# Kernel optimization log

Measured on AMD Instinct MI355X. Metric: run time of the kernel, lower is better.

The kernel has to match this reference:

```python
import jax, jax.numpy as jnp
import numpy as np

F_IN, F_H, N_A, N_B = 256, 512, 40, 4
N_GRAPHS, NODES_PER_GRAPH = 4096, 32
N_NODES = N_GRAPHS * NODES_PER_GRAPH
D_OUT = N_B + N_B * N_A  # 164
BN_EPS = 1e-5


def setup_inputs() -> dict:
    key = jax.random.key(0)
    ks = jax.random.split(key, 8)
    X = jax.random.normal(ks[0], (N_NODES, F_IN), dtype=jnp.float32)
    # fixed-size graphs: consistent NX / NX_rep pair
    NX = jnp.full((N_GRAPHS,), NODES_PER_GRAPH, dtype=jnp.int64)
    NX_rep = jnp.repeat(jnp.arange(N_GRAPHS, dtype=jnp.int64), NODES_PER_GRAPH)
    def kaiming(k, fo, fi):
        return jax.random.normal(k, (fo, fi), dtype=jnp.float32) * np.float32(1.0 / np.sqrt(fi))
    return {
        "X": X, "NX": NX, "NX_rep": NX_rep,
        "W_h": kaiming(ks[1], F_H, 2 * F_IN),          # linear_h (no bias)
        "g_h": jnp.ones((F_H,), jnp.float32), "b_h": jnp.zeros((F_H,), jnp.float32),
        "W_ht": kaiming(ks[2], F_H, F_IN),              # linear_h_t (no bias)
        "g_ht": jnp.ones((F_H,), jnp.float32), "b_ht": jnp.zeros((F_H,), jnp.float32),
        "W_x": kaiming(ks[3], D_OUT, F_H) * 0.1,        # linear_x
        "b_x": jnp.zeros((D_OUT,), jnp.float32),
        "W_xt": kaiming(ks[4], 1, F_H) * 0.1,           # linear_x_t
        "b_xt": jnp.zeros((1,), jnp.float32),
    }


def _batchnorm(x, gamma, beta):
    # BatchNorm1d in training mode: batch statistics, biased variance
    mean = jnp.mean(x, axis=0)
    var = jnp.var(x, axis=0)
    return (x - mean) * jax.lax.rsqrt(var + BN_EPS) * gamma + beta


def reference(X, NX, NX_rep, W_h, g_h, b_h, W_ht, g_ht, b_ht, W_x, b_x, W_xt, b_xt):
    n_graphs = NX.shape[0]
    # graph-level mean pooling via segment sum  -> [G, F_in]
    X_end = jax.ops.segment_sum(X, NX_rep, num_segments=n_graphs) / NX[:, None].astype(X.dtype)
    # concat node features with gathered graph context -> [N, 2*F_in]
    Xc = jnp.concatenate([X, X_end[NX_rep]], axis=1)
    X_h = jax.nn.relu(_batchnorm(Xc @ W_h.T, g_h, b_h))          # [N, F_h]
    X_h_end = jax.nn.relu(_batchnorm(X_end @ W_ht.T, g_ht, b_ht))  # [G, F_h]
    X_x = jnp.exp(X_h @ W_x.T + b_x)                              # [N, D_OUT]
    X_x_end = jnp.exp(X_h_end @ W_xt.T + b_xt)                    # [G, 1]
    # segmented softmax denominator (per graph, over all nodes x D_OUT + end logit)
    X_sum = jnp.sum(jax.ops.segment_sum(X_x, NX_rep, num_segments=n_graphs),
                    axis=-1, keepdims=True) + X_x_end             # [G, 1]
    X_softmax = X_x / X_sum[NX_rep]                               # [N, D_OUT]
    X_softmax_end = X_x_end / X_sum                               # [G, 1]
    connect = X_softmax[:, :N_B]                                  # [N, N_B]
    append = X_softmax[:, N_B:].reshape(-1, N_A, N_B)             # [N, N_A, N_B]
    end = X_softmax_end.squeeze(-1)                               # [G]
    return (append, connect, end)
```

## Files before the change

kernel.cpp:

```cpp
#include <hip/hip_runtime.h>
#include <hip/hip_bf16.h>

typedef __hip_bfloat16 bf16;
typedef __attribute__((ext_vector_type(8))) short bf16x8;
typedef __attribute__((ext_vector_type(4))) float f32x4;

#define N_NODES   131072
#define N_GRAPHS  4096
#define FIN       256
#define FH        512
#define NPAD      176
#define NREAL     164

#define OFF_XB     0UL
#define OFF_XEND   67108864UL
#define OFF_XENDB  71303168UL
#define OFF_W1A    73400320UL
#define OFF_BCAT   73662464UL
#define OFF_WXB    74186752UL
#define OFF_CCAT   74366976UL
#define OFF_H      91144192UL
#define OFF_STATS  225361920UL
#define OFF_COEF   225370112UL
#define OFF_XXE    225378304UL

__device__ __forceinline__ void gld_lds16(const void* g, void* l) {
  __builtin_amdgcn_global_load_lds(
      (const __attribute__((address_space(1))) void*)g,
      (__attribute__((address_space(3))) void*)l, 16, 0, 0);
}

__device__ __forceinline__ float bf2f(unsigned short u) {
  unsigned int x = ((unsigned int)u) << 16; float f;
  __builtin_memcpy(&f, &x, 4); return f;
}
__device__ __forceinline__ unsigned short f2bf(float f) {
  bf16 h = __float2bfloat16(f); unsigned short u;
  __builtin_memcpy(&u, &h, 2); return u;
}

__global__ __launch_bounds__(256) void k_wcast(
    const float* __restrict__ W_h, const float* __restrict__ W_ht,
    const float* __restrict__ W_x,
    bf16* __restrict__ W1a, bf16* __restrict__ Bcat, bf16* __restrict__ Wxb)
{
  int i = blockIdx.x * 256 + threadIdx.x;
  if (i < 512 * 512) {
    int of = i >> 9, ic = i & 511;
    float v = W_h[i];
    if (ic < 256) W1a[of * 256 + ic] = __float2bfloat16(v);
    else          Bcat[of * 256 + (ic - 256)] = __float2bfloat16(v);
  }
  if (i < 512 * 256) Bcat[512 * 256 + i] = __float2bfloat16(W_ht[i]);
  if (i < NPAD * 512) {
    int n = i >> 9;
    Wxb[i] = (n < NREAL) ? __float2bfloat16(W_x[i]) : __float2bfloat16(0.f);
  }
}

__global__ __launch_bounds__(256) void k_xend(
    const float* __restrict__ X, const int* __restrict__ NX,
    bf16* __restrict__ Xb, float* __restrict__ X_end, bf16* __restrict__ X_endb)
{
  int g = blockIdx.x;
  int f = threadIdx.x;
  float s = 0.f;
  long base = (long)g * 32 * FIN + f;
  #pragma unroll 4
  for (int n = 0; n < 32; ++n) {
    float v = X[base + (long)n * FIN];
    s += v;
    Xb[base + (long)n * FIN] = __float2bfloat16(v);
  }
  float m = s / (float)NX[g];
  X_end[g * FIN + f] = m;
  X_endb[g * FIN + f] = __float2bfloat16(m);
}

template <int MODE>
__global__ __launch_bounds__(256, 2) void gemm_tn(
    const bf16* __restrict__ A, int lda,
    const bf16* __restrict__ B, int ldb, int K,
    const float* __restrict__ Cterm, int ldct,
    float* __restrict__ Cout, int ldc,
    bf16* __restrict__ Hout, int nblk)
{
  const int bid = blockIdx.x;
  const int blkM = bid / nblk, blkN = bid % nblk;
  const int tid = threadIdx.x;
  const int w = tid >> 6, lane = tid & 63;
  const int wm = w >> 1, wn = w & 1;

  __shared__ __align__(16) bf16 lA[128 * 32];
  __shared__ __align__(16) bf16 lB[128 * 32];

  f32x4 acc[4][4] = {};

  const int rS = lane >> 2;
  const int cS = (lane & 3) * 8;
  const long baseA = (long)blkM * 128;
  const long baseB = (long)blkN * 128;

  for (int kk = 0; kk < K; kk += 32) {
    #pragma unroll
    for (int c = 0; c < 2; ++c) {
      int chunk = 2 * w + c;
      gld_lds16(A + (baseA + chunk * 16 + rS) * lda + kk + cS, &lA[chunk * 16 * 32]);
      gld_lds16(B + (baseB + chunk * 16 + rS) * ldb + kk + cS, &lB[chunk * 16 * 32]);
    }
    __syncthreads();
    bf16x8 a8[4], b8[4];
    #pragma unroll
    for (int t = 0; t < 4; ++t) {
      a8[t] = *(const bf16x8*)&lA[(wm * 64 + t * 16 + (lane & 15)) * 32 + (lane >> 4) * 8];
      b8[t] = *(const bf16x8*)&lB[(wn * 64 + t * 16 + (lane & 15)) * 32 + (lane >> 4) * 8];
    }
    #pragma unroll
    for (int tm = 0; tm < 4; ++tm)
      #pragma unroll
      for (int tn = 0; tn < 4; ++tn)
        acc[tm][tn] = __builtin_amdgcn_mfma_f32_16x16x32_bf16(a8[tm], b8[tn], acc[tm][tn], 0, 0, 0);
    __syncthreads();
  }

  const int rowq = (lane >> 4) * 4;
  const int coll = lane & 15;
  #pragma unroll
  for (int tm = 0; tm < 4; ++tm)
    #pragma unroll
    for (int tn = 0; tn < 4; ++tn)
      #pragma unroll
      for (int r = 0; r < 4; ++r) {
        long row = baseA + wm * 64 + tm * 16 + rowq + r;
        int col = (int)baseB + wn * 64 + tn * 16 + coll;
        if (MODE == 0) {
          Cout[row * ldc + col] = acc[tm][tn][r];
        } else {
          int g = (int)(row >> 5);
          float h = acc[tm][tn][r] + Cterm[(long)g * ldct + col];
          Hout[row * FH + col] = __float2bfloat16(h);
        }
      }
}

__global__ __launch_bounds__(256) void k_stats_main(
    const bf16* __restrict__ H, float* __restrict__ s1, float* __restrict__ s2)
{
  long r0 = (long)blockIdx.x * 128;
  int tid = threadIdx.x;
  #pragma unroll
  for (int cc = 0; cc < 2; ++cc) {
    int c = tid + cc * 256;
    float a = 0.f, b = 0.f;
    for (int r = 0; r < 128; ++r) {
      float v = bf2f(*(const unsigned short*)&H[(r0 + r) * FH + c]);
      a += v; b += v * v;
    }
    atomicAdd(&s1[c], a); atomicAdd(&s2[c], b);
  }
}

__global__ __launch_bounds__(256) void k_stats_end(
    const float* __restrict__ Ccat, float* __restrict__ s1, float* __restrict__ s2)
{
  long r0 = (long)blockIdx.x * 64;
  int tid = threadIdx.x;
  #pragma unroll
  for (int cc = 0; cc < 2; ++cc) {
    int c = tid + cc * 256;
    float a = 0.f, b = 0.f;
    for (int r = 0; r < 64; ++r) {
      float v = Ccat[(r0 + r) * 1024 + 512 + c];
      a += v; b += v * v;
    }
    atomicAdd(&s1[c], a); atomicAdd(&s2[c], b);
  }
}

__global__ __launch_bounds__(256) void k_finalize(
    const float* __restrict__ s1, const float* __restrict__ s2,
    const float* __restrict__ gam, const float* __restrict__ bet,
    float invN, float* __restrict__ a_s, float* __restrict__ c_s)
{
  int c = blockIdx.x * 256 + threadIdx.x;
  if (c < FH) {
    float mean = s1[c] * invN;
    float var = s2[c] * invN - mean * mean;
    float a = gam[c] / sqrtf(var + 1e-5f);
    a_s[c] = a;
    c_s[c] = bet[c] - mean * a;
  }
}

__global__ __launch_bounds__(256) void k_xxend(
    const float* __restrict__ Ccat, const float* __restrict__ at,
    const float* __restrict__ ct, const float* __restrict__ Wxt,
    const float* __restrict__ bxt, float* __restrict__ Xxe)
{
  int w = threadIdx.x >> 6, lane = threadIdx.x & 63;
  int g = blockIdx.x * 4 + w;
  const float* h = Ccat + (long)g * 1024 + 512;
  float acc = 0.f;
  #pragma unroll
  for (int i = 0; i < 8; ++i) {
    int j = lane + i * 64;
    float x = fmaxf(at[j] * h[j] + ct[j], 0.f);
    acc += x * Wxt[j];
  }
  #pragma unroll
  for (int off = 32; off; off >>= 1) acc += __shfl_xor(acc, off);
  if (lane == 0) Xxe[g] = expf(acc + bxt[0]);
}

__global__ __launch_bounds__(256) void k_transform(
    bf16* __restrict__ H, const float* __restrict__ a_s, const float* __restrict__ c_s)
{
  long i = ((long)blockIdx.x * 256 + threadIdx.x) * 8;
  int c0 = (int)(i & 511);
  uint4 d = *(const uint4*)((const char*)H + i * 2);
  unsigned short* u = (unsigned short*)&d;
  #pragma unroll
  for (int t = 0; t < 8; ++t) {
    float v = bf2f(u[t]);
    v = fmaxf(a_s[c0 + t] * v + c_s[c0 + t], 0.f);
    u[t] = f2bf(v);
  }
  *(uint4*)((char*)H + i * 2) = d;
}

__global__ __launch_bounds__(256, 2) void gemm2_softmax(
    const bf16* __restrict__ A2, const bf16* __restrict__ Wxb,
    const float* __restrict__ b_x, const float* __restrict__ Xxe,
    float* __restrict__ outA, float* __restrict__ outC, float* __restrict__ outE)
{
  const int blk = blockIdx.x;
  const int tid = threadIdx.x;
  const int w = tid >> 6, lane = tid & 63;

  __shared__ __align__(16) bf16 lA[128 * 32];
  __shared__ __align__(16) bf16 lB[NPAD * 32];

  f32x4 acc[2][11] = {};
  const int rS = lane >> 2;
  const int cS = (lane & 3) * 8;
  const long baseRow = (long)blk * 128;

  for (int kk = 0; kk < FH; kk += 32) {
    #pragma unroll
    for (int c = 0; c < 2; ++c) {
      int chunk = 2 * w + c;
      gld_lds16(A2 + (baseRow + chunk * 16 + rS) * FH + kk + cS, &lA[chunk * 16 * 32]);
    }
    for (int o = w; o < 11; o += 4)
      gld_lds16(Wxb + (o * 16 + rS) * FH + kk + cS, &lB[o * 16 * 32]);
    __syncthreads();

    bf16x8 a8[2], b8[11];
    #pragma unroll
    for (int t = 0; t < 2; ++t)
      a8[t] = *(const bf16x8*)&lA[(w * 32 + t * 16 + (lane & 15)) * 32 + (lane >> 4) * 8];
    #pragma unroll
    for (int t = 0; t < 11; ++t)
      b8[t] = *(const bf16x8*)&lB[(t * 16 + (lane & 15)) * 32 + (lane >> 4) * 8];
    #pragma unroll
    for (int tm = 0; tm < 2; ++tm)
      #pragma unroll
      for (int tn = 0; tn < 11; ++tn)
        acc[tm][tn] = __builtin_amdgcn_mfma_f32_16x16x32_bf16(a8[tm], b8[tn], acc[tm][tn], 0, 0, 0);
    __syncthreads();
  }

  const int rowq = (lane >> 4) * 4;
  const int coll = lane & 15;
  const int g = blk * 4 + w;
  float psum = 0.f;
  #pragma unroll
  for (int tn = 0; tn < 11; ++tn) {
    int col = tn * 16 + coll;
    bool valid = col < NREAL;
    float bx = valid ? b_x[col] : 0.f;
    #pragma unroll
    for (int tm = 0; tm < 2; ++tm)
      #pragma unroll
      for (int r = 0; r < 4; ++r) {
        float p = valid ? expf(acc[tm][tn][r] + bx) : 0.f;
        acc[tm][tn][r] = p;
        psum += p;
      }
  }
  #pragma unroll
  for (int off = 32; off; off >>= 1) psum += __shfl_xor(psum, off);
  float Xe = Xxe[g];
  float inv = 1.0f / (psum + Xe);
  if (lane == 0) outE[g] = Xe * inv;

  #pragma unroll
  for (int tn = 0; tn < 11; ++tn) {
    int col = tn * 16 + coll;
    if (col >= NREAL) continue;
    #pragma unroll
    for (int tm = 0; tm < 2; ++tm)
      #pragma unroll
      for (int r = 0; r < 4; ++r) {
        long row = baseRow + w * 32 + tm * 16 + rowq + r;
        float v = acc[tm][tn][r] * inv;
        if (col >= 4) outA[row * 160 + (col - 4)] = v;
        else          outC[row * 4 + col] = v;
      }
  }
}

extern "C" void kernel_launch(void* const* d_in, const int* in_sizes, int n_in,
                              void* d_out, int out_size, void* d_ws, size_t ws_size,
                              hipStream_t stream)
{
  const float* X    = (const float*)d_in[0];
  const int*   NX   = (const int*)d_in[1];
  const float* W_h  = (const float*)d_in[3];
  const float* g_h  = (const float*)d_in[4];
  const float* b_h  = (const float*)d_in[5];
  const float* W_ht = (const float*)d_in[6];
  const float* g_ht = (const float*)d_in[7];
  const float* b_ht = (const float*)d_in[8];
  const float* W_x  = (const float*)d_in[9];
  const float* b_x  = (const float*)d_in[10];
  const float* W_xt = (const float*)d_in[11];
  const float* b_xt = (const float*)d_in[12];

  char* ws = (char*)d_ws;
  bf16*  Xb    = (bf16*)(ws + OFF_XB);
  float* X_end = (float*)(ws + OFF_XEND);
  bf16*  X_endb= (bf16*)(ws + OFF_XENDB);
  bf16*  W1a   = (bf16*)(ws + OFF_W1A);
  bf16*  Bcat  = (bf16*)(ws + OFF_BCAT);
  bf16*  Wxb   = (bf16*)(ws + OFF_WXB);
  float* Ccat  = (float*)(ws + OFF_CCAT);
  bf16*  H     = (bf16*)(ws + OFF_H);
  float* stats = (float*)(ws + OFF_STATS);
  float* s1m = stats, *s2m = stats + 512, *s1e = stats + 1024, *s2e = stats + 1536;
  float* coef  = (float*)(ws + OFF_COEF);
  float* a_s = coef, *c_s = coef + 512, *at_s = coef + 1024, *ct_s = coef + 1536;
  float* Xxe   = (float*)(ws + OFF_XXE);

  float* outA = (float*)d_out;
  float* outC = outA + (long)N_NODES * 160;
  float* outE = outC + (long)N_NODES * 4;

  hipMemsetAsync(stats, 0, 4 * 512 * sizeof(float), stream);

  k_wcast<<<1024, 256, 0, stream>>>(W_h, W_ht, W_x, W1a, Bcat, Wxb);
  k_xend<<<N_GRAPHS, 256, 0, stream>>>(X, NX, Xb, X_end, X_endb);

  gemm_tn<0><<<256, 256, 0, stream>>>(X_endb, FIN, Bcat, FIN, FIN,
                                      nullptr, 0, Ccat, 1024, nullptr, 8);
  k_stats_end<<<64, 256, 0, stream>>>(Ccat, s1e, s2e);
  k_finalize<<<2, 256, 0, stream>>>(s1e, s2e, g_ht, b_ht, 1.f / 4096.f, at_s, ct_s);
  k_xxend<<<1024, 256, 0, stream>>>(Ccat, at_s, ct_s, W_xt, b_xt, Xxe);

  gemm_tn<1><<<4096, 256, 0, stream>>>(Xb, FIN, W1a, FIN, FIN,
                                       Ccat, 1024, nullptr, 0, H, 4);
  k_stats_main<<<1024, 256, 0, stream>>>(H, s1m, s2m);
  k_finalize<<<2, 256, 0, stream>>>(s1m, s2m, g_h, b_h, 1.f / 131072.f, a_s, c_s);
  k_transform<<<32768, 256, 0, stream>>>(H, a_s, c_s);

  gemm2_softmax<<<1024, 256, 0, stream>>>(H, Wxb, b_x, Xxe, outA, outC, outE);
}
```

Baseline: 482.9 us.

## Fuse batchnorm statistics and transform into GEMM epilogues and prologues

Removes the separate stats, finalize and transform kernels and the memset. BatchNorm sums are now reduced in the GEMM epilogues with shuffles and atomics, and the normalize+ReLU is applied while loading H into LDS in the final GEMM. The main GEMM reads fp32 X directly and converts it to bf16 on the fly, so the bf16 copy of X is no longer written. Fewer kernels and less HBM traffic, at the cost of register-staged A loads in place of direct-to-LDS loads, plus redundant per-block coefficient computation.

```diff
diff --git a/kernel.cpp b/kernel.cpp
--- a/kernel.cpp
+++ b/kernel.cpp
@@ -12,17 +12,14 @@
 #define NPAD      176
 #define NREAL     164
 
-#define OFF_XB     0UL
-#define OFF_XEND   67108864UL
-#define OFF_XENDB  71303168UL
-#define OFF_W1A    73400320UL
-#define OFF_BCAT   73662464UL
-#define OFF_WXB    74186752UL
-#define OFF_CCAT   74366976UL
-#define OFF_H      91144192UL
-#define OFF_STATS  225361920UL
-#define OFF_COEF   225370112UL
-#define OFF_XXE    225378304UL
+#define OFF_XENDB  0UL
+#define OFF_W1A    2097152UL
+#define OFF_BCAT   2359296UL
+#define OFF_WXB    2883584UL
+#define OFF_STATS  3063808UL
+#define OFF_XXE    3072000UL
+#define OFF_CCAT   3088384UL
+#define OFF_H      19865600UL
 
 __device__ __forceinline__ void gld_lds16(const void* g, void* l) {
   __builtin_amdgcn_global_load_lds(
@@ -42,9 +39,11 @@
 __global__ __launch_bounds__(256) void k_wcast(
     const float* __restrict__ W_h, const float* __restrict__ W_ht,
     const float* __restrict__ W_x,
-    bf16* __restrict__ W1a, bf16* __restrict__ Bcat, bf16* __restrict__ Wxb)
+    bf16* __restrict__ W1a, bf16* __restrict__ Bcat, bf16* __restrict__ Wxb,
+    float* __restrict__ stats)
 {
   int i = blockIdx.x * 256 + threadIdx.x;
+  if (i < 2048) stats[i] = 0.f;
   if (i < 512 * 512) {
     int of = i >> 9, ic = i & 511;
     float v = W_h[i];
@@ -60,53 +59,58 @@
 
 __global__ __launch_bounds__(256) void k_xend(
     const float* __restrict__ X, const int* __restrict__ NX,
-    bf16* __restrict__ Xb, float* __restrict__ X_end, bf16* __restrict__ X_endb)
+    bf16* __restrict__ X_endb)
 {
   int g = blockIdx.x;
-  int f = threadIdx.x;
-  float s = 0.f;
-  long base = (long)g * 32 * FIN + f;
-  #pragma unroll 4
-  for (int n = 0; n < 32; ++n) {
-    float v = X[base + (long)n * FIN];
-    s += v;
-    Xb[base + (long)n * FIN] = __float2bfloat16(v);
-  }
-  float m = s / (float)NX[g];
-  X_end[g * FIN + f] = m;
-  X_endb[g * FIN + f] = __float2bfloat16(m);
-}
-
-template <int MODE>
-__global__ __launch_bounds__(256, 2) void gemm_tn(
-    const bf16* __restrict__ A, int lda,
-    const bf16* __restrict__ B, int ldb, int K,
-    const float* __restrict__ Cterm, int ldct,
-    float* __restrict__ Cout, int ldc,
-    bf16* __restrict__ Hout, int nblk)
+  int t = threadIdx.x;
+  int cg = t & 63;
+  int rg = t >> 6;
+  const float* Xg = X + (long)g * 32 * FIN;
+  float4 s = {0.f, 0.f, 0.f, 0.f};
+  #pragma unroll
+  for (int r = 0; r < 8; ++r) {
+    float4 v = *(const float4*)(Xg + (rg * 8 + r) * FIN + cg * 4);
+    s.x += v.x; s.y += v.y; s.z += v.z; s.w += v.w;
+  }
+  __shared__ float4 red[256];
+  red[t] = s;
+  __syncthreads();
+  if (t < 64) {
+    float4 a = red[t], b = red[t + 64], c = red[t + 128], d = red[t + 192];
+    float inv = 1.f / (float)NX[g];
+    float4 m = {(a.x + b.x + c.x + d.x) * inv, (a.y + b.y + c.y + d.y) * inv,
+                (a.z + b.z + c.z + d.z) * inv, (a.w + b.w + c.w + d.w) * inv};
+    ushort4 u = {f2bf(m.x), f2bf(m.y), f2bf(m.z), f2bf(m.w)};
+    *(ushort4*)(X_endb + (long)g * FIN + t * 4) = u;
+  }
+}
+
+__global__ __launch_bounds__(256, 2) void gemm0(
+    const bf16* __restrict__ A, const bf16* __restrict__ B,
+    float* __restrict__ Cout, float* __restrict__ s1e, float* __restrict__ s2e)
 {
   const int bid = blockIdx.x;
-  const int blkM = bid / nblk, blkN = bid % nblk;
+  const int blkM = bid >> 3, blkN = bid & 7;
   const int tid = threadIdx.x;
   const int w = tid >> 6, lane = tid & 63;
   const int wm = w >> 1, wn = w & 1;
 
   __shared__ __align__(16) bf16 lA[128 * 32];
   __shared__ __align__(16) bf16 lB[128 * 32];
+  __shared__ float sred[2][2][128];
 
   f32x4 acc[4][4] = {};
-
   const int rS = lane >> 2;
   const int cS = (lane & 3) * 8;
   const long baseA = (long)blkM * 128;
   const long baseB = (long)blkN * 128;
 
-  for (int kk = 0; kk < K; kk += 32) {
+  for (int kk = 0; kk < FIN; kk += 32) {
     #pragma unroll
     for (int c = 0; c < 2; ++c) {
       int chunk = 2 * w + c;
-      gld_lds16(A + (baseA + chunk * 16 + rS) * lda + kk + cS, &lA[chunk * 16 * 32]);
-      gld_lds16(B + (baseB + chunk * 16 + rS) * ldb + kk + cS, &lB[chunk * 16 * 32]);
+      gld_lds16(A + (baseA + chunk * 16 + rS) * FIN + kk + cS, &lA[chunk * 16 * 32]);
+      gld_lds16(B + (baseB + chunk * 16 + rS) * FIN + kk + cS, &lB[chunk * 16 * 32]);
     }
     __syncthreads();
     bf16x8 a8[4], b8[4];
@@ -125,6 +129,7 @@
 
   const int rowq = (lane >> 4) * 4;
   const int coll = lane & 15;
+  float p1[4] = {0.f, 0.f, 0.f, 0.f}, p2[4] = {0.f, 0.f, 0.f, 0.f};
   #pragma unroll
   for (int tm = 0; tm < 4; ++tm)
     #pragma unroll
@@ -133,78 +138,53 @@
       for (int r = 0; r < 4; ++r) {
         long row = baseA + wm * 64 + tm * 16 + rowq + r;
         int col = (int)baseB + wn * 64 + tn * 16 + coll;
-        if (MODE == 0) {
-          Cout[row * ldc + col] = acc[tm][tn][r];
-        } else {
-          int g = (int)(row >> 5);
-          float h = acc[tm][tn][r] + Cterm[(long)g * ldct + col];
-          Hout[row * FH + col] = __float2bfloat16(h);
-        }
-      }
-}
-
-__global__ __launch_bounds__(256) void k_stats_main(
-    const bf16* __restrict__ H, float* __restrict__ s1, float* __restrict__ s2)
-{
-  long r0 = (long)blockIdx.x * 128;
+        float v = acc[tm][tn][r];
+        Cout[row * 1024 + col] = v;
+        p1[tn] += v; p2[tn] += v * v;
+      }
+
+  if (blkN >= 4) {
+    #pragma unroll
+    for (int tn = 0; tn < 4; ++tn) {
+      float q1 = p1[tn], q2 = p2[tn];
+      q1 += __shfl_xor(q1, 16); q1 += __shfl_xor(q1, 32);
+      q2 += __shfl_xor(q2, 16); q2 += __shfl_xor(q2, 32);
+      if (lane < 16) {
+        sred[wm][0][wn * 64 + tn * 16 + lane] = q1;
+        sred[wm][1][wn * 64 + tn * 16 + lane] = q2;
+      }
+    }
+    __syncthreads();
+    int st = tid >> 7, c = tid & 127;
+    float v = sred[0][st][c] + sred[1][st][c];
+    atomicAdd((st ? s2e : s1e) + (blkN - 4) * 128 + c, v);
+  }
+}
+
+__global__ __launch_bounds__(256) void k_xxend(
+    const float* __restrict__ Ccat, const float* __restrict__ s1e,
+    const float* __restrict__ s2e, const float* __restrict__ g_ht,
+    const float* __restrict__ b_ht, const float* __restrict__ Wxt,
+    const float* __restrict__ bxt, float* __restrict__ Xxe)
+{
+  __shared__ float aL[512], cL[512];
   int tid = threadIdx.x;
   #pragma unroll
-  for (int cc = 0; cc < 2; ++cc) {
-    int c = tid + cc * 256;
-    float a = 0.f, b = 0.f;
-    for (int r = 0; r < 128; ++r) {
-      float v = bf2f(*(const unsigned short*)&H[(r0 + r) * FH + c]);
-      a += v; b += v * v;
-    }
-    atomicAdd(&s1[c], a); atomicAdd(&s2[c], b);
-  }
-}
-
-__global__ __launch_bounds__(256) void k_stats_end(
-    const float* __restrict__ Ccat, float* __restrict__ s1, float* __restrict__ s2)
-{
-  long r0 = (long)blockIdx.x * 64;
-  int tid = threadIdx.x;
-  #pragma unroll
-  for (int cc = 0; cc < 2; ++cc) {
-    int c = tid + cc * 256;
-    float a = 0.f, b = 0.f;
-    for (int r = 0; r < 64; ++r) {
-      float v = Ccat[(r0 + r) * 1024 + 512 + c];
-      a += v; b += v * v;
-    }
-    atomicAdd(&s1[c], a); atomicAdd(&s2[c], b);
-  }
-}
-
-__global__ __launch_bounds__(256) void k_finalize(
-    const float* __restrict__ s1, const float* __restrict__ s2,
-    const float* __restrict__ gam, const float* __restrict__ bet,
-    float invN, float* __restrict__ a_s, float* __restrict__ c_s)
-{
-  int c = blockIdx.x * 256 + threadIdx.x;
-  if (c < FH) {
-    float mean = s1[c] * invN;
-    float var = s2[c] * invN - mean * mean;
-    float a = gam[c] / sqrtf(var + 1e-5f);
-    a_s[c] = a;
-    c_s[c] = bet[c] - mean * a;
-  }
-}
-
-__global__ __launch_bounds__(256) void k_xxend(
-    const float* __restrict__ Ccat, const float* __restrict__ at,
-    const float* __restrict__ ct, const float* __restrict__ Wxt,
-    const float* __restrict__ bxt, float* __restrict__ Xxe)
-{
-  int w = threadIdx.x >> 6, lane = threadIdx.x & 63;
+  for (int i = tid; i < 512; i += 256) {
+    float mean = s1e[i] * 2.44140625e-4f;
+    float var = s2e[i] * 2.44140625e-4f - mean * mean;
+    float a = g_ht[i] / sqrtf(var + 1e-5f);
+    aL[i] = a; cL[i] = b_ht[i] - mean * a;
+  }
+  __syncthreads();
+  int w = tid >> 6, lane = tid & 63;
   int g = blockIdx.x * 4 + w;
   const float* h = Ccat + (long)g * 1024 + 512;
   float acc = 0.f;
   #pragma unroll
   for (int i = 0; i < 8; ++i) {
     int j = lane + i * 64;
-    float x = fmaxf(at[j] * h[j] + ct[j], 0.f);
+    float x = fmaxf(aL[j] * h[j] + cL[j], 0.f);
     acc += x * Wxt[j];
   }
   #pragma unroll
@@ -212,24 +192,96 @@
   if (lane == 0) Xxe[g] = expf(acc + bxt[0]);
 }
 
-__global__ __launch_bounds__(256) void k_transform(
-    bf16* __restrict__ H, const float* __restrict__ a_s, const float* __restrict__ c_s)
-{
-  long i = ((long)blockIdx.x * 256 + threadIdx.x) * 8;
-  int c0 = (int)(i & 511);
-  uint4 d = *(const uint4*)((const char*)H + i * 2);
-  unsigned short* u = (unsigned short*)&d;
-  #pragma unroll
-  for (int t = 0; t < 8; ++t) {
-    float v = bf2f(u[t]);
-    v = fmaxf(a_s[c0 + t] * v + c_s[c0 + t], 0.f);
-    u[t] = f2bf(v);
-  }
-  *(uint4*)((char*)H + i * 2) = d;
-}
-
-__global__ __launch_bounds__(256, 2) void gemm2_softmax(
-    const bf16* __restrict__ A2, const bf16* __restrict__ Wxb,
+__global__ __launch_bounds__(256, 2) void gemm1(
+    const float* __restrict__ X, const bf16* __restrict__ W1a,
+    const float* __restrict__ Ccat, bf16* __restrict__ H,
+    float* __restrict__ s1m, float* __restrict__ s2m)
+{
+  const int bid = blockIdx.x;
+  const int blkM = bid >> 2, blkN = bid & 3;
+  const int tid = threadIdx.x;
+  const int w = tid >> 6, lane = tid & 63;
+  const int wm = w >> 1, wn = w & 1;
+
+  __shared__ __align__(16) bf16 lA[128 * 32];
+  __shared__ __align__(16) bf16 lB[128 * 32];
+  __shared__ float sred[2][2][128];
+
+  f32x4 acc[4][4] = {};
+  const int rS = lane >> 2;
+  const int cS = (lane & 3) * 8;
+  const long baseA = (long)blkM * 128;
+  const long baseB = (long)blkN * 128;
+
+  for (int kk = 0; kk < FIN; kk += 32) {
+    #pragma unroll
+    for (int c = 0; c < 2; ++c) {
+      int chunk = 2 * w + c;
+      gld_lds16(W1a + (baseB + chunk * 16 + rS) * FIN + kk + cS, &lB[chunk * 16 * 32]);
+    }
+    #pragma unroll
+    for (int c = 0; c < 2; ++c) {
+      int chunk = 2 * w + c;
+      const float* src = X + (baseA + chunk * 16 + rS) * FIN + kk + cS;
+      float4 v0 = *(const float4*)src;
+      float4 v1 = *(const float4*)(src + 4);
+      ushort4 u0 = {f2bf(v0.x), f2bf(v0.y), f2bf(v0.z), f2bf(v0.w)};
+      ushort4 u1 = {f2bf(v1.x), f2bf(v1.y), f2bf(v1.z), f2bf(v1.w)};
+      uint4 pk; __builtin_memcpy(&pk, &u0, 8); __builtin_memcpy(((char*)&pk) + 8, &u1, 8);
+      *(uint4*)&lA[(chunk * 16 + rS) * 32 + cS] = pk;
+    }
+    __syncthreads();
+    bf16x8 a8[4], b8[4];
+    #pragma unroll
+    for (int t = 0; t < 4; ++t) {
+      a8[t] = *(const bf16x8*)&lA[(wm * 64 + t * 16 + (lane & 15)) * 32 + (lane >> 4) * 8];
+      b8[t] = *(const bf16x8*)&lB[(wn * 64 + t * 16 + (lane & 15)) * 32 + (lane >> 4) * 8];
+    }
+    #pragma unroll
+    for (int tm = 0; tm < 4; ++tm)
+      #pragma unroll
+      for (int tn = 0; tn < 4; ++tn)
+        acc[tm][tn] = __builtin_amdgcn_mfma_f32_16x16x32_bf16(a8[tm], b8[tn], acc[tm][tn], 0, 0, 0);
+    __syncthreads();
+  }
+
+  const int rowq = (lane >> 4) * 4;
+  const int coll = lane & 15;
+  float p1[4] = {0.f, 0.f, 0.f, 0.f}, p2[4] = {0.f, 0.f, 0.f, 0.f};
+  #pragma unroll
+  for (int tm = 0; tm < 4; ++tm)
+    #pragma unroll
+    for (int tn = 0; tn < 4; ++tn)
+      #pragma unroll
+      for (int r = 0; r < 4; ++r) {
+        long row = baseA + wm * 64 + tm * 16 + rowq + r;
+        int col = (int)baseB + wn * 64 + tn * 16 + coll;
+        int g = (int)(row >> 5);
+        float h = acc[tm][tn][r] + Ccat[(long)g * 1024 + col];
+        H[row * FH + col] = __float2bfloat16(h);
+        p1[tn] += h; p2[tn] += h * h;
+      }
+
+  #pragma unroll
+  for (int tn = 0; tn < 4; ++tn) {
+    float q1 = p1[tn], q2 = p2[tn];
+    q1 += __shfl_xor(q1, 16); q1 += __shfl_xor(q1, 32);
+    q2 += __shfl_xor(q2, 16); q2 += __shfl_xor(q2, 32);
+    if (lane < 16) {
+      sred[wm][0][wn * 64 + tn * 16 + lane] = q1;
+      sred[wm][1][wn * 64 + tn * 16 + lane] = q2;
+    }
+  }
+  __syncthreads();
+  int st = tid >> 7, c = tid & 127;
+  float v = sred[0][st][c] + sred[1][st][c];
+  atomicAdd((st ? s2m : s1m) + (int)baseB + c, v);
+}
+
+__global__ __launch_bounds__(256, 2) void gemm2(
+    const bf16* __restrict__ Hraw, const bf16* __restrict__ Wxb,
+    const float* __restrict__ s1m, const float* __restrict__ s2m,
+    const float* __restrict__ g_h, const float* __restrict__ b_h,
     const float* __restrict__ b_x, const float* __restrict__ Xxe,
     float* __restrict__ outA, float* __restrict__ outC, float* __restrict__ outE)
 {
@@ -239,6 +291,16 @@
 
   __shared__ __align__(16) bf16 lA[128 * 32];
   __shared__ __align__(16) bf16 lB[NPAD * 32];
+  __shared__ float aL[512], cL[512];
+
+  #pragma unroll
+  for (int i = tid; i < 512; i += 256) {
+    float mean = s1m[i] * 7.62939453125e-6f;
+    float var = s2m[i] * 7.62939453125e-6f - mean * mean;
+    float a = g_h[i] / sqrtf(var + 1e-5f);
+    aL[i] = a; cL[i] = b_h[i] - mean * a;
+  }
+  __syncthreads();
 
   f32x4 acc[2][11] = {};
   const int rS = lane >> 2;
@@ -246,13 +308,30 @@
   const long baseRow = (long)blk * 128;
 
   for (int kk = 0; kk < FH; kk += 32) {
+    for (int o = w; o < 11; o += 4)
+      gld_lds16(Wxb + (o * 16 + rS) * FH + kk + cS, &lB[o * 16 * 32]);
+
+    f32x4 a0 = *(const f32x4*)&aL[kk + cS];
+    f32x4 a1 = *(const f32x4*)&aL[kk + cS + 4];
+    f32x4 c0 = *(const f32x4*)&cL[kk + cS];
+    f32x4 c1 = *(const f32x4*)&cL[kk + cS + 4];
     #pragma unroll
     for (int c = 0; c < 2; ++c) {
       int chunk = 2 * w + c;
-      gld_lds16(A2 + (baseRow + chunk * 16 + rS) * FH + kk + cS, &lA[chunk * 16 * 32]);
-    }
-    for (int o = w; o < 11; o += 4)
-      gld_lds16(Wxb + (o * 16 + rS) * FH + kk + cS, &lB[o * 16 * 32]);
+      uint4 raw = *(const uint4*)(Hraw + (baseRow + chunk * 16 + rS) * FH + kk + cS);
+      unsigned short* u = (unsigned short*)&raw;
+      #pragma unroll
+      for (int j = 0; j < 4; ++j) {
+        float v = bf2f(u[j]);
+        u[j] = f2bf(fmaxf(a0[j] * v + c0[j], 0.f));
+      }
+      #pragma unroll
+      for (int j = 0; j < 4; ++j) {
+        float v = bf2f(u[4 + j]);
+        u[4 + j] = f2bf(fmaxf(a1[j] * v + c1[j], 0.f));
+      }
+      *(uint4*)&lA[(chunk * 16 + rS) * 32 + cS] = raw;
+    }
     __syncthreads();
 
     bf16x8 a8[2], b8[11];
@@ -328,40 +407,24 @@
   const float* b_xt = (const float*)d_in[12];
 
   char* ws = (char*)d_ws;
-  bf16*  Xb    = (bf16*)(ws + OFF_XB);
-  float* X_end = (float*)(ws + OFF_XEND);
   bf16*  X_endb= (bf16*)(ws + OFF_XENDB);
   bf16*  W1a   = (bf16*)(ws + OFF_W1A);
   bf16*  Bcat  = (bf16*)(ws + OFF_BCAT);
   bf16*  Wxb   = (bf16*)(ws + OFF_WXB);
+  float* stats = (float*)(ws + OFF_STATS);
+  float* s1m = stats, *s2m = stats + 512, *s1e = stats + 1024, *s2e = stats + 1536;
+  float* Xxe   = (float*)(ws + OFF_XXE);
   float* Ccat  = (float*)(ws + OFF_CCAT);
   bf16*  H     = (bf16*)(ws + OFF_H);
-  float* stats = (float*)(ws + OFF_STATS);
-  float* s1m = stats, *s2m = stats + 512, *s1e = stats + 1024, *s2e = stats + 1536;
-  float* coef  = (float*)(ws + OFF_COEF);
-  float* a_s = coef, *c_s = coef + 512, *at_s = coef + 1024, *ct_s = coef + 1536;
-  float* Xxe   = (float*)(ws + OFF_XXE);
 
   float* outA = (float*)d_out;
   float* outC = outA + (long)N_NODES * 160;
   float* outE = outC + (long)N_NODES * 4;
 
-  hipMemsetAsync(stats, 0, 4 * 512 * sizeof(float), stream);
-
-  k_wcast<<<1024, 256, 0, stream>>>(W_h, W_ht, W_x, W1a, Bcat, Wxb);
-  k_xend<<<N_GRAPHS, 256, 0, stream>>>(X, NX, Xb, X_end, X_endb);
-
-  gemm_tn<0><<<256, 256, 0, stream>>>(X_endb, FIN, Bcat, FIN, FIN,
-                                      nullptr, 0, Ccat, 1024, nullptr, 8);
-  k_stats_end<<<64, 256, 0, stream>>>(Ccat, s1e, s2e);
-  k_finalize<<<2, 256, 0, stream>>>(s1e, s2e, g_ht, b_ht, 1.f / 4096.f, at_s, ct_s);
-  k_xxend<<<1024, 256, 0, stream>>>(Ccat, at_s, ct_s, W_xt, b_xt, Xxe);
-
-  gemm_tn<1><<<4096, 256, 0, stream>>>(Xb, FIN, W1a, FIN, FIN,
-                                       Ccat, 1024, nullptr, 0, H, 4);
-  k_stats_main<<<1024, 256, 0, stream>>>(H, s1m, s2m);
-  k_finalize<<<2, 256, 0, stream>>>(s1m, s2m, g_h, b_h, 1.f / 131072.f, a_s, c_s);
-  k_transform<<<32768, 256, 0, stream>>>(H, a_s, c_s);
-
-  gemm2_softmax<<<1024, 256, 0, stream>>>(H, Wxb, b_x, Xxe, outA, outC, outE);
-}
+  k_wcast<<<1024, 256, 0, stream>>>(W_h, W_ht, W_x, W1a, Bcat, Wxb, stats);
+  k_xend<<<N_GRAPHS, 256, 0, stream>>>(X, NX, X_endb);
+  gemm0<<<256, 256, 0, stream>>>(X_endb, Bcat, Ccat, s1e, s2e);
+  k_xxend<<<1024, 256, 0, stream>>>(Ccat, s1e, s2e, g_ht, b_ht, W_xt, b_xt, Xxe);
+  gemm1<<<4096, 256, 0, stream>>>(X, W1a, Ccat, H, s1m, s2m);
+  gemm2<<<1024, 256, 0, stream>>>(H, Wxb, s1m, s2m, g_h, b_h, b_x, Xxe, outA, outC, outE);
+}
```

Result: faster. 427.6 us (-11.5%).
